# Kernel tuning notes

Measured on AMD Instinct MI355X. Metric: run time of the kernel, lower is better.

The kernel has to match this reference:

```python
import jax, jax.numpy as jnp
import numpy as np

EOS = 1e-10
N_NODES = 100000
N_EDGES = 1600000
IN_DIM = 256
HID = 64
ALPHA = 0.1
TEMP = 1.0
BIAS = 1e-4


def setup_inputs() -> dict:
    key = jax.random.key(0)
    k1, k2, k3, k4, k5 = jax.random.split(key, 5)
    features = jax.random.normal(k1, (N_NODES, IN_DIM), dtype=jnp.float32)
    edges = jax.random.randint(k2, (2, N_EDGES), 0, N_NODES, dtype=jnp.int64)
    noise = jax.random.uniform(k3, (N_EDGES,), dtype=jnp.float32)
    # params: embedding Linear(input_dim, hidden) and edge_mlp Linear(2*hidden, 1)
    W_emb = jax.random.normal(k4, (IN_DIM, HID), dtype=jnp.float32) / np.sqrt(IN_DIM)
    b_emb = jnp.zeros((HID,), dtype=jnp.float32)
    W_edge = jax.random.normal(k5, (2 * HID,), dtype=jnp.float32) / np.sqrt(2 * HID)
    b_edge = jnp.zeros((), dtype=jnp.float32)
    return {"features": features, "edges": edges, "noise": noise,
            "W_emb": W_emb, "b_emb": b_emb, "W_edge": W_edge, "b_edge": b_edge}


def _edge_weight_norm_both(src, dst, w, n_nodes):
    # DGL EdgeWeightNorm(norm='both'): w_e / sqrt(outdeg_w(src) * indeg_w(dst))
    deg_out = jax.ops.segment_sum(w, src, num_segments=n_nodes)
    deg_in = jax.ops.segment_sum(w, dst, num_segments=n_nodes)
    return w / jnp.sqrt(deg_out[src] * deg_in[dst])


def reference(features, edges, noise, W_emb, b_emb, W_edge, b_edge):
    src, dst = edges[0], edges[1]
    E = src.shape[0]
    # node embedding: relu(Linear(features))
    h = jax.nn.relu(features @ W_emb + b_emb)  # [N, H]
    # edge score: edge_mlp(cat(h[u], h[v])) symmetrized.
    # split W_edge -> score = h[u]@W1 + h[v]@W2 + b  (avoids materializing concat)
    p1 = h @ W_edge[:HID]   # [N]
    p2 = h @ W_edge[HID:]   # [N]
    s1 = p1[src] + p2[dst] + b_edge
    s2 = p1[dst] + p2[src] + b_edge
    raw = (s1 + s2) * 0.5   # [E]
    # gumbel sigmoid sampling
    eps = (BIAS - (1.0 - BIAS)) * noise + (1.0 - BIAS)
    gate = jnp.log(eps) - jnp.log1p(-eps)
    weights_lp = jax.nn.sigmoid((gate + raw) / TEMP)  # [E]
    weights_hp = 1.0 - weights_lp
    # weight_to_adj: add self loops with weight 1, then EdgeWeightNorm 'both'
    loop = jnp.arange(N_NODES, dtype=src.dtype)
    src_f = jnp.concatenate([src, loop])
    dst_f = jnp.concatenate([dst, loop])
    ones_n = jnp.ones((N_NODES,), dtype=weights_lp.dtype)
    w_lp_full = jnp.concatenate([weights_lp, ones_n]) + EOS
    w_lp_norm = _edge_weight_norm_both(src_f, dst_f, w_lp_full, N_NODES)
    w_hp_full = jnp.concatenate([weights_hp, ones_n]) + EOS
    w_hp_norm = _edge_weight_norm_both(src_f, dst_f, w_hp_full, N_NODES)
    w_hp_norm = w_hp_norm * (-ALPHA)
    w_hp_norm = w_hp_norm.at[E:].set(1.0)  # self-loop weights forced to 1
    return (w_lp_norm, w_hp_norm, weights_lp, weights_hp)
```

## Files before the change

### kernel.cpp

```cpp
#include <hip/hip_runtime.h>
#include <hip/hip_bf16.h>
#include <math.h>

#define N_NODESC 100000
#define N_EDGESC 1600000
#define IN_DIMC 256
#define HIDC 64
#define ALPHAC 0.1f
#define BIASC 1e-4f
#define EOSC 1e-10f

#define MC (N_EDGESC + N_NODESC)
#define NBUCK 100
#define BSHIFT 10
#define BMASK 1023
#define BCAP 17000u
#define W20SCALE 1048576.0f
#define W20INV (1.0f / 1048576.0f)
#define SUMMASK ((1ull << 40) - 1)
#define CNTONE (1ull << 40)
#define EPB 8

typedef __attribute__((ext_vector_type(8))) short short8;
typedef __attribute__((ext_vector_type(4))) float f32x4;

#define WT_STRIDE 264

__device__ inline void load_edge(const int* __restrict__ edges, int e, int is64,
                                 int& src, int& dst) {
    if (is64) {
        const int2 a = ((const int2*)edges)[e];
        const int2 b = ((const int2*)edges)[N_EDGESC + e];
        src = a.x; dst = b.x;
    } else {
        src = edges[e];
        dst = edges[N_EDGESC + e];
    }
}

__device__ inline short pkbf(float x) {
    union { __hip_bfloat16 b; short s; } u;
    u.b = __float2bfloat16(x);
    return u.s;
}

__global__ __launch_bounds__(256, 3) void node_kernel(
    const float* __restrict__ features,
    const float* __restrict__ W_emb,
    const float* __restrict__ b_emb,
    const float* __restrict__ W_edge,
    const int* __restrict__ edges,
    float* __restrict__ q,
    unsigned* __restrict__ cursor,
    int* __restrict__ flag) {
    __shared__ __align__(16) short Wt[HIDC * WT_STRIDE];
    const int tid = threadIdx.x;
    if (blockIdx.x == 0) {
        if (tid == 0) {
            int z = 0;
            #pragma unroll
            for (int i = 0; i < 16; ++i) z |= edges[2 * i + 1];
            *flag = (z == 0) ? 1 : 0;
        }
        if (tid < 2 * NBUCK) cursor[tid] = 0u;
    }
    {
        const float4* Wg = (const float4*)W_emb;
        #pragma unroll
        for (int i = 0; i < 16; ++i) {
            const int f4 = tid + 256 * i;
            const float4 g = Wg[f4];
            const int flat = 4 * f4;
            const int k = flat >> 6;
            const int j0 = flat & 63;
            Wt[(j0 + 0) * WT_STRIDE + k] = pkbf(g.x);
            Wt[(j0 + 1) * WT_STRIDE + k] = pkbf(g.y);
            Wt[(j0 + 2) * WT_STRIDE + k] = pkbf(g.z);
            Wt[(j0 + 3) * WT_STRIDE + k] = pkbf(g.w);
        }
    }
    const int lane = tid & 63;
    const int wave = tid >> 6;
    const int quad = lane >> 4;
    const int m = lane & 15;
    f32x4 accA[4], accB[4];
    float wsum4[4];
    #pragma unroll
    for (int nt = 0; nt < 4; ++nt) {
        const int j = m + 16 * nt;
        const float b = b_emb[j];
        accA[nt] = (f32x4){b, b, b, b};
        accB[nt] = (f32x4){b, b, b, b};
        wsum4[nt] = W_edge[j] + W_edge[HIDC + j];
    }
    __syncthreads();

    const int node0A = blockIdx.x * 128 + wave * 16;
    const int node0B = node0A + 64;
    const float* frA = features + (size_t)min(node0A + m, N_NODESC - 1) * IN_DIMC;
    const float* frB = features + (size_t)min(node0B + m, N_NODESC - 1) * IN_DIMC;

    #pragma unroll
    for (int ks = 0; ks < 8; ++ks) {
        const int kk = ks * 32 + quad * 8;
        const float4 fa0 = *(const float4*)(frA + kk);
        const float4 fb0 = *(const float4*)(frA + kk + 4);
        const float4 fa1 = *(const float4*)(frB + kk);
        const float4 fb1 = *(const float4*)(frB + kk + 4);
        short8 afA, afB;
        afA[0] = pkbf(fa0.x); afA[1] = pkbf(fa0.y);
        afA[2] = pkbf(fa0.z); afA[3] = pkbf(fa0.w);
        afA[4] = pkbf(fb0.x); afA[5] = pkbf(fb0.y);
        afA[6] = pkbf(fb0.z); afA[7] = pkbf(fb0.w);
        afB[0] = pkbf(fa1.x); afB[1] = pkbf(fa1.y);
        afB[2] = pkbf(fa1.z); afB[3] = pkbf(fa1.w);
        afB[4] = pkbf(fb1.x); afB[5] = pkbf(fb1.y);
        afB[6] = pkbf(fb1.z); afB[7] = pkbf(fb1.w);
        #pragma unroll
        for (int nt = 0; nt < 4; ++nt) {
            const short8 bf =
                *(const short8*)&Wt[(m + 16 * nt) * WT_STRIDE + kk];
            accA[nt] = __builtin_amdgcn_mfma_f32_16x16x32_bf16(afA, bf, accA[nt],
                                                               0, 0, 0);
            accB[nt] = __builtin_amdgcn_mfma_f32_16x16x32_bf16(afB, bf, accB[nt],
                                                               0, 0, 0);
        }
    }

    #pragma unroll
    for (int r = 0; r < 4; ++r) {
        float sA = 0.f, sB = 0.f;
        #pragma unroll
        for (int nt = 0; nt < 4; ++nt) {
            sA = fmaf(fmaxf(accA[nt][r], 0.f), wsum4[nt], sA);
            sB = fmaf(fmaxf(accB[nt][r], 0.f), wsum4[nt], sB);
        }
        sA += __shfl_xor(sA, 1); sA += __shfl_xor(sA, 2);
        sA += __shfl_xor(sA, 4); sA += __shfl_xor(sA, 8);
        sB += __shfl_xor(sB, 1); sB += __shfl_xor(sB, 2);
        sB += __shfl_xor(sB, 4); sB += __shfl_xor(sB, 8);
        if (m == 0) {
            const int nA = node0A + quad * 4 + r;
            const int nB = node0B + quad * 4 + r;
            if (nA < N_NODESC) q[nA] = sA;
            if (nB < N_NODESC) q[nB] = sB;
        }
    }
}

__global__ __launch_bounds__(256) void edge_scatter(
    const int* __restrict__ edges,
    const float* __restrict__ noise,
    const float* __restrict__ b_edge,
    const float* __restrict__ q,
    unsigned* __restrict__ cursor,
    float* __restrict__ out,
    const int* __restrict__ flag) {
    __shared__ unsigned hist[2][4][NBUCK];
    __shared__ unsigned wbase[2][4][NBUCK];
    const int tid = threadIdx.x;
    const int wave = tid >> 6;
    for (int i = tid; i < 2 * 4 * NBUCK; i += 256)
        ((unsigned*)hist)[i] = 0u;
    __syncthreads();
    const int is64 = *flag;
    const float be = b_edge[0];
    const int e0 = blockIdx.x * (256 * EPB) + tid;

    int sA[EPB], dA[EPB];
    #pragma unroll
    for (int i = 0; i < EPB; ++i) {
        const int e = e0 + i * 256;
        sA[i] = -1;
        if (e < N_EDGESC) load_edge(edges, e, is64, sA[i], dA[i]);
    }
    float qs[EPB], qd[EPB];
    #pragma unroll
    for (int i = 0; i < EPB; ++i) {
        if (sA[i] >= 0) { qs[i] = q[sA[i]]; qd[i] = q[dA[i]]; }
    }
    float wlpA[EPB];
    unsigned rkS[EPB], rkD[EPB];
    #pragma unroll
    for (int i = 0; i < EPB; ++i) {
        if (sA[i] >= 0) {
            const int e = e0 + i * 256;
            const float raw = 0.5f * (qs[i] + qd[i]) + be;
            const float u = noise[e];
            const float eps = (BIASC - (1.0f - BIASC)) * u + (1.0f - BIASC);
            const float gate = logf(eps) - log1pf(-eps);
            const float wlp = 1.0f / (1.0f + expf(-(gate + raw)));
            wlpA[i] = wlp;
            out[2 * MC + e] = wlp;
            out[2 * MC + N_EDGESC + e] = 1.0f - wlp;
            rkS[i] = atomicAdd(&hist[0][wave][sA[i] >> BSHIFT], 1u);
            rkD[i] = atomicAdd(&hist[1][wave][dA[i] >> BSHIFT], 1u);
        }
    }
    __syncthreads();
    if (tid < NBUCK) {
        const unsigned h0 = hist[0][0][tid], h1 = hist[0][1][tid];
        const unsigned h2 = hist[0][2][tid], h3 = hist[0][3][tid];
        const unsigned base = atomicAdd(&cursor[tid], h0 + h1 + h2 + h3);
        wbase[0][0][tid] = base;
        wbase[0][1][tid] = base + h0;
        wbase[0][2][tid] = base + h0 + h1;
        wbase[0][3][tid] = base + h0 + h1 + h2;
    } else if (tid >= 128 && tid < 128 + NBUCK) {
        const int b = tid - 128;
        const unsigned h0 = hist[1][0][b], h1 = hist[1][1][b];
        const unsigned h2 = hist[1][2][b], h3 = hist[1][3][b];
        const unsigned base = atomicAdd(&cursor[NBUCK + b], h0 + h1 + h2 + h3);
        wbase[1][0][b] = base;
        wbase[1][1][b] = base + h0;
        wbase[1][2][b] = base + h0 + h1;
        wbase[1][3][b] = base + h0 + h1 + h2;
    }
    __syncthreads();
    unsigned* recS = (unsigned*)out;
    unsigned* recD = (unsigned*)out + MC;
    #pragma unroll
    for (int i = 0; i < EPB; ++i) {
        if (sA[i] >= 0) {
            const int s = sA[i], d = dA[i];
            const unsigned w20 =
                min((unsigned)(wlpA[i] * W20SCALE + 0.5f), 0xFFFFFu);
            const unsigned pS = wbase[0][wave][s >> BSHIFT] + rkS[i];
            const unsigned pD = wbase[1][wave][d >> BSHIFT] + rkD[i];
            if (pS < BCAP)
                recS[(unsigned)(s >> BSHIFT) * BCAP + pS] =
                    ((unsigned)(s & BMASK) << 20) | w20;
            if (pD < BCAP)
                recD[(unsigned)(d >> BSHIFT) * BCAP + pD] =
                    ((unsigned)(d & BMASK) << 20) | w20;
        }
    }
}

__global__ __launch_bounds__(512) void gather_kernel(
    const float* __restrict__ out,
    const unsigned* __restrict__ cursor,
    float2* __restrict__ rS,
    float2* __restrict__ rD) {
    __shared__ unsigned long long table[1024];
    const int bid = blockIdx.x;
    const int isD = bid >= NBUCK;
    const int bkt = isD ? bid - NBUCK : bid;
    const unsigned* rec = (const unsigned*)out + (isD ? MC : 0) +
                          (unsigned)bkt * BCAP;
    const unsigned cnt = min(cursor[isD ? NBUCK + bkt : bkt], BCAP);
    const int tid = threadIdx.x;
    table[tid] = 0ull;
    table[tid + 512] = 0ull;
    __syncthreads();
    for (unsigned i = tid; i < cnt; i += 512) {
        const unsigned r = rec[i];
        atomicAdd(&table[r >> 20], CNTONE | (unsigned long long)(r & 0xFFFFFu));
    }
    __syncthreads();
    float2* dstp = isD ? rD : rS;
    const int node0 = bkt << BSHIFT;
    #pragma unroll
    for (int j = 0; j < 2; ++j) {
        const int local = tid + 512 * j;
        const int node = node0 + local;
        if (node < N_NODESC) {
            const unsigned long long a = table[local];
            const float sum = (float)(a & SUMMASK) * W20INV;
            const float cf = (float)(a >> 40);
            float2 r;
            r.x = rsqrtf(1.0f + sum);
            r.y = rsqrtf(1.0f + cf - sum);
            dstp[node] = r;
        }
    }
}

__global__ __launch_bounds__(256) void final_kernel(
    const int* __restrict__ edges,
    const float2* __restrict__ rS,
    const float2* __restrict__ rD,
    float* __restrict__ out,
    const int* __restrict__ flag) {
    const int tid = threadIdx.x;
    const int i0 = blockIdx.x * 1024 + tid;
    const int is64 = *flag;
    int sA[4], dA[4];
    float wl[4], wh[4];
    #pragma unroll
    for (int j = 0; j < 4; ++j) {
        const int i = i0 + j * 256;
        sA[j] = -1;
        if (i < N_EDGESC) {
            load_edge(edges, i, is64, sA[j], dA[j]);
        } else if (i < MC) {
            sA[j] = dA[j] = i - N_EDGESC;
        }
    }
    #pragma unroll
    for (int j = 0; j < 4; ++j) {
        const int i = i0 + j * 256;
        if (i < N_EDGESC) {
            wl[j] = out[2 * MC + i] + EOSC;
            wh[j] = out[2 * MC + N_EDGESC + i] + EOSC;
        } else {
            wl[j] = 1.0f + EOSC;
        }
    }
    float2 a[4], b[4];
    #pragma unroll
    for (int j = 0; j < 4; ++j) {
        if (sA[j] >= 0) { a[j] = rS[sA[j]]; b[j] = rD[dA[j]]; }
    }
    #pragma unroll
    for (int j = 0; j < 4; ++j) {
        const int i = i0 + j * 256;
        if (sA[j] >= 0) {
            out[i] = wl[j] * a[j].x * b[j].x;
            out[MC + i] = (i < N_EDGESC)
                              ? -ALPHAC * wh[j] * a[j].y * b[j].y
                              : 1.0f;
        }
    }
}

extern "C" void kernel_launch(void* const* d_in, const int* in_sizes, int n_in,
                              void* d_out, int out_size, void* d_ws, size_t ws_size,
                              hipStream_t stream) {
    const float* features = (const float*)d_in[0];
    const int* edges      = (const int*)d_in[1];
    const float* noise    = (const float*)d_in[2];
    const float* W_emb    = (const float*)d_in[3];
    const float* b_emb    = (const float*)d_in[4];
    const float* W_edge   = (const float*)d_in[5];
    const float* b_edge   = (const float*)d_in[6];
    float* out = (float*)d_out;
    char* ws = (char*)d_ws;

    float* q = (float*)ws;
    float2* rS = (float2*)(ws + 400000);
    float2* rD = (float2*)(ws + 1200000);
    int* flag = (int*)(ws + 3600000);
    unsigned* cursor = (unsigned*)(ws + 3600004);

    node_kernel<<<782, 256, 0, stream>>>(features, W_emb, b_emb, W_edge, edges,
                                         q, cursor, flag);
    edge_scatter<<<(N_EDGESC + 256 * EPB - 1) / (256 * EPB), 256, 0, stream>>>(
        edges, noise, b_edge, q, cursor, out, flag);
    gather_kernel<<<2 * NBUCK, 512, 0, stream>>>(out, cursor, rS, rD);
    final_kernel<<<(MC + 1023) / 1024, 256, 0, stream>>>(edges, rS, rD, out, flag);
}
```

Baseline: 266.8 us.

## Replace bucketed scatter/gather degree computation with direct global 64-bit atomics

Drops the LDS-histogram bucketing, record writes and separate gather kernel, and instead accumulates packed count+weight degrees per node with global 64-bit atomicAdd in the edge kernel. The final kernel reads the packed degrees and computes the rsqrt normalizations per edge, and derives the high-pass weight from the low-pass one instead of reloading it. This removes one launch and the intermediate record traffic, at the cost of millions of random-address global atomics and repeated rsqrt work.

```diff
diff --git a/kernel.cpp b/kernel.cpp
--- a/kernel.cpp
+++ b/kernel.cpp
@@ -11,10 +11,6 @@
 #define EOSC 1e-10f
 
 #define MC (N_EDGESC + N_NODESC)
-#define NBUCK 100
-#define BSHIFT 10
-#define BMASK 1023
-#define BCAP 17000u
 #define W20SCALE 1048576.0f
 #define W20INV (1.0f / 1048576.0f)
 #define SUMMASK ((1ull << 40) - 1)
@@ -51,18 +47,19 @@
     const float* __restrict__ W_edge,
     const int* __restrict__ edges,
     float* __restrict__ q,
-    unsigned* __restrict__ cursor,
+    unsigned long long* __restrict__ deg,
     int* __restrict__ flag) {
     __shared__ __align__(16) short Wt[HIDC * WT_STRIDE];
     const int tid = threadIdx.x;
-    if (blockIdx.x == 0) {
-        if (tid == 0) {
-            int z = 0;
-            #pragma unroll
-            for (int i = 0; i < 16; ++i) z |= edges[2 * i + 1];
-            *flag = (z == 0) ? 1 : 0;
-        }
-        if (tid < 2 * NBUCK) cursor[tid] = 0u;
+    {
+        const int gid = blockIdx.x * 256 + tid;
+        if (gid < 2 * N_NODESC) deg[gid] = 0ull;
+    }
+    if (blockIdx.x == 0 && tid == 0) {
+        int z = 0;
+        #pragma unroll
+        for (int i = 0; i < 16; ++i) z |= edges[2 * i + 1];
+        *flag = (z == 0) ? 1 : 0;
     }
     {
         const float4* Wg = (const float4*)W_emb;
@@ -148,21 +145,16 @@
     }
 }
 
-__global__ __launch_bounds__(256) void edge_scatter(
+__global__ __launch_bounds__(256) void edge_kernel(
     const int* __restrict__ edges,
     const float* __restrict__ noise,
     const float* __restrict__ b_edge,
     const float* __restrict__ q,
-    unsigned* __restrict__ cursor,
+    unsigned long long* __restrict__ degS,
+    unsigned long long* __restrict__ degD,
     float* __restrict__ out,
     const int* __restrict__ flag) {
-    __shared__ unsigned hist[2][4][NBUCK];
-    __shared__ unsigned wbase[2][4][NBUCK];
     const int tid = threadIdx.x;
-    const int wave = tid >> 6;
-    for (int i = tid; i < 2 * 4 * NBUCK; i += 256)
-        ((unsigned*)hist)[i] = 0u;
-    __syncthreads();
     const int is64 = *flag;
     const float be = b_edge[0];
     const int e0 = blockIdx.x * (256 * EPB) + tid;
@@ -180,7 +172,6 @@
         if (sA[i] >= 0) { qs[i] = q[sA[i]]; qd[i] = q[dA[i]]; }
     }
     float wlpA[EPB];
-    unsigned rkS[EPB], rkD[EPB];
     #pragma unroll
     for (int i = 0; i < EPB; ++i) {
         if (sA[i] >= 0) {
@@ -193,93 +184,24 @@
             wlpA[i] = wlp;
             out[2 * MC + e] = wlp;
             out[2 * MC + N_EDGESC + e] = 1.0f - wlp;
-            rkS[i] = atomicAdd(&hist[0][wave][sA[i] >> BSHIFT], 1u);
-            rkD[i] = atomicAdd(&hist[1][wave][dA[i] >> BSHIFT], 1u);
-        }
-    }
-    __syncthreads();
-    if (tid < NBUCK) {
-        const unsigned h0 = hist[0][0][tid], h1 = hist[0][1][tid];
-        const unsigned h2 = hist[0][2][tid], h3 = hist[0][3][tid];
-        const unsigned base = atomicAdd(&cursor[tid], h0 + h1 + h2 + h3);
-        wbase[0][0][tid] = base;
-        wbase[0][1][tid] = base + h0;
-        wbase[0][2][tid] = base + h0 + h1;
-        wbase[0][3][tid] = base + h0 + h1 + h2;
-    } else if (tid >= 128 && tid < 128 + NBUCK) {
-        const int b = tid - 128;
-        const unsigned h0 = hist[1][0][b], h1 = hist[1][1][b];
-        const unsigned h2 = hist[1][2][b], h3 = hist[1][3][b];
-        const unsigned base = atomicAdd(&cursor[NBUCK + b], h0 + h1 + h2 + h3);
-        wbase[1][0][b] = base;
-        wbase[1][1][b] = base + h0;
-        wbase[1][2][b] = base + h0 + h1;
-        wbase[1][3][b] = base + h0 + h1 + h2;
-    }
-    __syncthreads();
-    unsigned* recS = (unsigned*)out;
-    unsigned* recD = (unsigned*)out + MC;
+        }
+    }
     #pragma unroll
     for (int i = 0; i < EPB; ++i) {
         if (sA[i] >= 0) {
-            const int s = sA[i], d = dA[i];
             const unsigned w20 =
                 min((unsigned)(wlpA[i] * W20SCALE + 0.5f), 0xFFFFFu);
-            const unsigned pS = wbase[0][wave][s >> BSHIFT] + rkS[i];
-            const unsigned pD = wbase[1][wave][d >> BSHIFT] + rkD[i];
-            if (pS < BCAP)
-                recS[(unsigned)(s >> BSHIFT) * BCAP + pS] =
-                    ((unsigned)(s & BMASK) << 20) | w20;
-            if (pD < BCAP)
-                recD[(unsigned)(d >> BSHIFT) * BCAP + pD] =
-                    ((unsigned)(d & BMASK) << 20) | w20;
-        }
-    }
-}
-
-__global__ __launch_bounds__(512) void gather_kernel(
-    const float* __restrict__ out,
-    const unsigned* __restrict__ cursor,
-    float2* __restrict__ rS,
-    float2* __restrict__ rD) {
-    __shared__ unsigned long long table[1024];
-    const int bid = blockIdx.x;
-    const int isD = bid >= NBUCK;
-    const int bkt = isD ? bid - NBUCK : bid;
-    const unsigned* rec = (const unsigned*)out + (isD ? MC : 0) +
-                          (unsigned)bkt * BCAP;
-    const unsigned cnt = min(cursor[isD ? NBUCK + bkt : bkt], BCAP);
-    const int tid = threadIdx.x;
-    table[tid] = 0ull;
-    table[tid + 512] = 0ull;
-    __syncthreads();
-    for (unsigned i = tid; i < cnt; i += 512) {
-        const unsigned r = rec[i];
-        atomicAdd(&table[r >> 20], CNTONE | (unsigned long long)(r & 0xFFFFFu));
-    }
-    __syncthreads();
-    float2* dstp = isD ? rD : rS;
-    const int node0 = bkt << BSHIFT;
-    #pragma unroll
-    for (int j = 0; j < 2; ++j) {
-        const int local = tid + 512 * j;
-        const int node = node0 + local;
-        if (node < N_NODESC) {
-            const unsigned long long a = table[local];
-            const float sum = (float)(a & SUMMASK) * W20INV;
-            const float cf = (float)(a >> 40);
-            float2 r;
-            r.x = rsqrtf(1.0f + sum);
-            r.y = rsqrtf(1.0f + cf - sum);
-            dstp[node] = r;
+            const unsigned long long v = CNTONE | (unsigned long long)w20;
+            atomicAdd(&degS[sA[i]], v);
+            atomicAdd(&degD[dA[i]], v);
         }
     }
 }
 
 __global__ __launch_bounds__(256) void final_kernel(
     const int* __restrict__ edges,
-    const float2* __restrict__ rS,
-    const float2* __restrict__ rD,
+    const unsigned long long* __restrict__ degS,
+    const unsigned long long* __restrict__ degD,
     float* __restrict__ out,
     const int* __restrict__ flag) {
     const int tid = threadIdx.x;
@@ -301,25 +223,36 @@
     for (int j = 0; j < 4; ++j) {
         const int i = i0 + j * 256;
         if (i < N_EDGESC) {
-            wl[j] = out[2 * MC + i] + EOSC;
-            wh[j] = out[2 * MC + N_EDGESC + i] + EOSC;
+            const float wlp = out[2 * MC + i];
+            wl[j] = wlp + EOSC;
+            wh[j] = (1.0f - wlp) + EOSC;
         } else {
             wl[j] = 1.0f + EOSC;
         }
     }
-    float2 a[4], b[4];
-    #pragma unroll
-    for (int j = 0; j < 4; ++j) {
-        if (sA[j] >= 0) { a[j] = rS[sA[j]]; b[j] = rD[dA[j]]; }
+    unsigned long long aS[4], aD[4];
+    #pragma unroll
+    for (int j = 0; j < 4; ++j) {
+        if (sA[j] >= 0) { aS[j] = degS[sA[j]]; aD[j] = degD[dA[j]]; }
     }
     #pragma unroll
     for (int j = 0; j < 4; ++j) {
         const int i = i0 + j * 256;
         if (sA[j] >= 0) {
-            out[i] = wl[j] * a[j].x * b[j].x;
-            out[MC + i] = (i < N_EDGESC)
-                              ? -ALPHAC * wh[j] * a[j].y * b[j].y
-                              : 1.0f;
+            const float sumS = (float)(aS[j] & SUMMASK) * W20INV;
+            const float cS = (float)(aS[j] >> 40);
+            const float sumD = (float)(aD[j] & SUMMASK) * W20INV;
+            const float cD = (float)(aD[j] >> 40);
+            const float rSx = rsqrtf(1.0f + sumS);
+            const float rDx = rsqrtf(1.0f + sumD);
+            out[i] = wl[j] * rSx * rDx;
+            if (i < N_EDGESC) {
+                const float rSy = rsqrtf(1.0f + cS - sumS);
+                const float rDy = rsqrtf(1.0f + cD - sumD);
+                out[MC + i] = -ALPHAC * wh[j] * rSy * rDy;
+            } else {
+                out[MC + i] = 1.0f;
+            }
         }
     }
 }
@@ -338,15 +271,14 @@
     char* ws = (char*)d_ws;
 
     float* q = (float*)ws;
-    float2* rS = (float2*)(ws + 400000);
-    float2* rD = (float2*)(ws + 1200000);
-    int* flag = (int*)(ws + 3600000);
-    unsigned* cursor = (unsigned*)(ws + 3600004);
+    unsigned long long* degS = (unsigned long long*)(ws + 400000);
+    unsigned long long* degD = (unsigned long long*)(ws + 1200000);
+    int* flag = (int*)(ws + 2000000);
 
     node_kernel<<<782, 256, 0, stream>>>(features, W_emb, b_emb, W_edge, edges,
-                                         q, cursor, flag);
-    edge_scatter<<<(N_EDGESC + 256 * EPB - 1) / (256 * EPB), 256, 0, stream>>>(
-        edges, noise, b_edge, q, cursor, out, flag);
-    gather_kernel<<<2 * NBUCK, 512, 0, stream>>>(out, cursor, rS, rD);
-    final_kernel<<<(MC + 1023) / 1024, 256, 0, stream>>>(edges, rS, rD, out, flag);
-}
+                                         q, degS, flag);
+    edge_kernel<<<(N_EDGESC + 256 * EPB - 1) / (256 * EPB), 256, 0, stream>>>(
+        edges, noise, b_edge, q, degS, degD, out, flag);
+    final_kernel<<<(MC + 1023) / 1024, 256, 0, stream>>>(edges, degS, degD, out,
+                                                         flag);
+}
```

New measurement: 367.4 us. 1.38x slower.
